# Performance work log

Measured on AMD Instinct MI355X. Metric: run time of the kernel, lower is better.

The kernel has to match this reference:

```python
import jax, jax.numpy as jnp
import numpy as np

EMBED = 1024
HEADS = 16
HEAD_DIM = EMBED // HEADS


def setup_inputs() -> dict:
    key = jax.random.key(0)
    ks = jax.random.split(key, 8)
    N, S = 4, 2048
    inp = {
        "values": jax.random.normal(ks[0], (N, S, EMBED), jnp.float32),
        "keys": jax.random.normal(ks[1], (N, S, EMBED), jnp.float32),
        "queries": jax.random.normal(ks[2], (N, S, EMBED), jnp.float32),
        "mask": jnp.ones((N, S), jnp.int32),  # unused by the original forward
        # learned params (torch Linear: y = x @ W.T + b)
        "Wv": jax.random.normal(ks[3], (HEAD_DIM, HEAD_DIM), jnp.float32) / np.sqrt(HEAD_DIM),
        "Wk": jax.random.normal(ks[4], (HEAD_DIM, HEAD_DIM), jnp.float32) / np.sqrt(HEAD_DIM),
        "Wq": jax.random.normal(ks[5], (HEAD_DIM, HEAD_DIM), jnp.float32) / np.sqrt(HEAD_DIM),
        "Wo": jax.random.normal(ks[6], (EMBED, EMBED), jnp.float32) / np.sqrt(EMBED),
        "bo": jax.random.normal(ks[7], (EMBED,), jnp.float32) * 0.01,
    }
    return inp


def reference(values, keys, queries, mask, Wv, Wk, Wq, Wo, bo):
    N, S, _ = queries.shape
    # reshape to (N, len, heads, head_dim)
    v = values.reshape(N, S, HEADS, HEAD_DIM)
    k = keys.reshape(N, S, HEADS, HEAD_DIM)
    q = queries.reshape(N, S, HEADS, HEAD_DIM)
    # per-head linear projections (weights shared across heads), y = x @ W.T
    v = jnp.einsum('nlhd,ed->nlhe', v, Wv)
    k = jnp.einsum('nlhd,ed->nlhe', k, Wk)
    q = jnp.einsum('nlhd,ed->nlhe', q, Wq)
    # attention scores scaled by sqrt(embed_size), faithful to original
    scores = jnp.einsum('nqhd,nkhd->nhqk', q, k) / jnp.sqrt(jnp.float32(EMBED))
    attn = jax.nn.softmax(scores, axis=3)
    out = jnp.einsum('nhql,nlhd->nqhd', attn, v).reshape(N, S, EMBED)
    return out @ Wo.T + bo
```

## Files before the change

kernel.cpp:

```cpp
#include <hip/hip_runtime.h>


using f32x4  = __attribute__((ext_vector_type(4))) float;
using f32x16 = __attribute__((ext_vector_type(16))) float;
using bf16x8 = __attribute__((ext_vector_type(8))) __bf16;
using u32x4  = __attribute__((ext_vector_type(4))) unsigned int;
using u16x8  = __attribute__((ext_vector_type(8))) unsigned short;
typedef unsigned short u16;
typedef unsigned int   u32;
typedef unsigned long long u64;

#define SEQ 2048
#define EMB 1024
#define NHEADS 16
#define HDIM 64
#define NBATCH 4
#define NH 64

__device__ __forceinline__ u16 f2bf(float f) {
  u32 u = __builtin_bit_cast(u32, f);
  return (u16)((u + 0x7fffu + ((u >> 16) & 1u)) >> 16);
}

__device__ __forceinline__ u32 cvtpk_bf16(float a, float b) {
  u32 d;
  asm("v_cvt_pk_bf16_f32 %0, %1, %2" : "=v"(d) : "v"(a), "v"(b));
  return d;
}

__device__ __forceinline__ f32x4 mfma16(bf16x8 a, bf16x8 b, f32x4 c) {
  return __builtin_amdgcn_mfma_f32_16x16x32_bf16(a, b, c, 0, 0, 0);
}

__device__ __forceinline__ f32x16 mfma32(bf16x8 a, bf16x8 b, f32x16 c) {
  return __builtin_amdgcn_mfma_f32_32x32x16_bf16(a, b, c, 0, 0, 0);
}

__device__ __forceinline__ bf16x8 cvt8(f32x4 a, f32x4 b) {
  u32x4 r;
  r[0] = cvtpk_bf16(a[0], a[1]);
  r[1] = cvtpk_bf16(a[2], a[3]);
  r[2] = cvtpk_bf16(b[0], b[1]);
  r[3] = cvtpk_bf16(b[2], b[3]);
  return __builtin_bit_cast(bf16x8, r);
}

__device__ __forceinline__ float fexp2(float x) {
#if __has_builtin(__builtin_amdgcn_exp2f)
  return __builtin_amdgcn_exp2f(x);
#else
  return __expf(x * 0.6931471805599453f);
#endif
}

__device__ __forceinline__ void swap_words(u32 a, u32 b, int hi, u32& wlo, u32& whi) {
#if __has_builtin(__builtin_amdgcn_permlane32_swap)
  (void)hi;
  auto rr = __builtin_amdgcn_permlane32_swap((int)a, (int)b, false, false);
  wlo = (u32)rr[0];
  whi = (u32)rr[1];
#else
  u32 pa = (u32)__shfl_xor((int)a, 32);
  u32 pb = (u32)__shfl_xor((int)b, 32);
  wlo = hi ? pb : a;
  whi = hi ? b : pa;
#endif
}

__global__ __launch_bounds__(256) void proj_kernel(
    const float* __restrict__ Xq, const float* __restrict__ Xk, const float* __restrict__ Xv,
    const float* __restrict__ Wq, const float* __restrict__ Wk, const float* __restrict__ Wv,
    u16* __restrict__ Qp, u16* __restrict__ Kp, u16* __restrict__ Vp)
{
  int which = blockIdx.y;
  const float* X = which == 0 ? Xq : (which == 1 ? Xk : Xv);
  const float* W = which == 0 ? Wq : (which == 1 ? Wk : Wv);
  u16* Out = which == 0 ? Qp : (which == 1 ? Kp : Vp);
  float wscale = which == 0 ? 0.045084220027780106f : 1.0f;

  __shared__ u16 Osm[64 * 72];

  int t = threadIdx.x;
  int w = t >> 6, l = t & 63, l15 = l & 15, grp = l >> 4;
  int g0 = blockIdx.x * 64;

  bf16x8 wf[4][2];
#pragma unroll
  for (int nt = 0; nt < 4; nt++) {
    int c = nt * 16 + l15;
#pragma unroll
    for (int dc = 0; dc < 2; dc++) {
      const float* p = W + c * 64 + dc * 32 + grp * 8;
      f32x4 a = *(const f32x4*)p;
      f32x4 b = *(const f32x4*)(p + 4);
      a *= wscale; b *= wscale;
      wf[nt][dc] = cvt8(a, b);
    }
  }
  int grow = g0 + w * 16 + l15;
  const float* xr = X + (long)grow * 64;
  bf16x8 af[2];
#pragma unroll
  for (int dc = 0; dc < 2; dc++) {
    f32x4 a = *(const f32x4*)(xr + dc * 32 + grp * 8);
    f32x4 b = *(const f32x4*)(xr + dc * 32 + grp * 8 + 4);
    af[dc] = cvt8(a, b);
  }
  f32x4 acc[4] = {};
#pragma unroll
  for (int dc = 0; dc < 2; dc++)
#pragma unroll
    for (int nt = 0; nt < 4; nt++)
      acc[nt] = mfma16(af[dc], wf[nt][dc], acc[nt]);

#pragma unroll
  for (int r = 0; r < 4; r++)
#pragma unroll
    for (int nt = 0; nt < 4; nt++)
      Osm[(w * 16 + grp * 4 + r) * 72 + nt * 16 + l15] = f2bf(acc[nt][r]);

  int rl = t >> 2, qtr = t & 3;
  const char* srcp = (const char*)Osm + rl * 144 + qtr * 32;
  u32x4 v0 = *(const u32x4*)srcp;
  u32x4 v1 = *(const u32x4*)(srcp + 16);
  int g = g0 + rl;
  int n = g >> 15, s = (g >> 4) & 2047, h = g & 15;
  char* dstp = (char*)(Out + (((long)(n * NHEADS + h) * SEQ + s) << 6)) + qtr * 32;
  *(u32x4*)dstp = v0;
  *(u32x4*)(dstp + 16) = v1;
}

__global__ __launch_bounds__(256) void transpose_v(
    const u16* __restrict__ Vp, u16* __restrict__ Vt)
{
  int st = blockIdx.x;
  int nh = blockIdx.y;
  __shared__ u16 Vs[64 * 65];
  int t = threadIdx.x;
  const u16* src = Vp + ((long)nh * SEQ + st * 64) * 64;
#pragma unroll
  for (int p = 0; p < 2; p++) {
    int row = p * 32 + (t >> 3);
    int c0 = (t & 7) * 8;
    u32x4 u = *(const u32x4*)(src + row * 64 + c0);
    u16x8 v = __builtin_bit_cast(u16x8, u);
#pragma unroll
    for (int j = 0; j < 8; j++) Vs[(c0 + j) * 65 + row] = v[j];
  }
  __syncthreads();
  int e = t >> 2, k0 = (t & 3) * 16;
  u16x8 lo, hi;
#pragma unroll
  for (int j = 0; j < 8; j++) { lo[j] = Vs[e * 65 + k0 + j]; hi[j] = Vs[e * 65 + k0 + 8 + j]; }
  u16* dst = Vt + ((long)nh * 64 + e) * SEQ + st * 64 + k0;
  *(u32x4*)dst = __builtin_bit_cast(u32x4, lo);
  *(u32x4*)(dst + 8) = __builtin_bit_cast(u32x4, hi);
}

__global__ __launch_bounds__(256) void conv_wo(
    const float* __restrict__ Wo, u16* __restrict__ Wob)
{
  int i = (blockIdx.x * 256 + threadIdx.x) * 4;
  f32x4 v = *(const f32x4*)(Wo + i);
  u32 w0 = cvtpk_bf16(v[0], v[1]);
  u32 w1 = cvtpk_bf16(v[2], v[3]);
  u64 pk = (u64)w0 | ((u64)w1 << 32);
  *(u64*)(Wob + i) = pk;
}


#define LDV(off) __builtin_bit_cast(bf16x8, *(const u32x4*)(smem + (off)))

#define ATTN_STEP(CUROFF, DOSTAGE, DOPREF) do {                            \
    f32x16 zz = {};                                                        \
    f32x16 s0, s1;                                                         \
    __builtin_amdgcn_s_setprio(1);                                         \
    {                                                                      \
      bf16x8 kf0 = LDV(koff[0] + (CUROFF));                                \
      bf16x8 kf1 = LDV(koff[1] + (CUROFF));                                \
      s0 = mfma32(kf0, qf[0], zz);                                         \
      s1 = mfma32(kf1, qf[0], zz);                                         \
    }                                                                      \
    _Pragma("unroll")                                                      \
    for (int dc = 1; dc < 4; dc++) {                                       \
      bf16x8 kf0 = LDV(koff[dc * 2 + 0] + (CUROFF));                       \
      bf16x8 kf1 = LDV(koff[dc * 2 + 1] + (CUROFF));                       \
      s0 = mfma32(kf0, qf[dc], s0);                                        \
      s1 = mfma32(kf1, qf[dc], s1);                                        \
    }                                                                      \
    __builtin_amdgcn_s_setprio(0);                                         \
    if (DOSTAGE) {                                                         \
      *(u32x4*)(smem + sphys0 + ((CUROFF) ^ 16384)) = kreg[0];             \
      *(u32x4*)(smem + sphys1 + ((CUROFF) ^ 16384)) = kreg[1];             \
      *(u32x4*)(smem + sphys0 + 8192 + ((CUROFF) ^ 16384)) = vreg[0];      \
      *(u32x4*)(smem + sphys1 + 8192 + ((CUROFF) ^ 16384)) = vreg[1];      \
      if (DOPREF) {                                                        \
        kreg[0] = *(const u32x4*)kp0; kp0 += 8192;                         \
        kreg[1] = *(const u32x4*)kp1; kp1 += 8192;                         \
        vreg[0] = *(const u32x4*)vp0; vp0 += 128;                          \
        vreg[1] = *(const u32x4*)vp1; vp1 += 128;                          \
      }                                                                    \
    }                                                                      \
                                    \
    _Pragma("unroll")                                                      \
    for (int r = 0; r < 16; r++) s0[r] = fexp2(s0[r]);                     \
    _Pragma("unroll")                                                      \
    for (int r = 0; r < 16; r++) s1[r] = fexp2(s1[r]);                     \
    { f32x16 ss = s0 + s1;                                                 \
      f32x4 q4 = { ss[0]+ss[4], ss[1]+ss[5], ss[2]+ss[6], ss[3]+ss[7] };   \
      f32x4 q5 = { ss[8]+ss[12], ss[9]+ss[13], ss[10]+ss[14], ss[11]+ss[15] }; \
      f32x4 q6 = q4 + q5;                                                  \
      lrun += (q6[0] + q6[1]) + (q6[2] + q6[3]); }                         \
              \
    bf16x8 pB[4];                                                          \
    { u32 xw[8], wq[16];                                                   \
      _Pragma("unroll")                                                    \
      for (int i = 0; i < 8; i++) xw[i] = cvtpk_bf16(s0[2*i], s0[2*i+1]);  \
      swap_words(xw[0], xw[2], hi, wq[0], wq[2]);                          \
      swap_words(xw[1], xw[3], hi, wq[1], wq[3]);                          \
      swap_words(xw[4], xw[6], hi, wq[4], wq[6]);                          \
      swap_words(xw[5], xw[7], hi, wq[5], wq[7]);                          \
      _Pragma("unroll")                                                    \
      for (int i = 0; i < 8; i++) xw[i] = cvtpk_bf16(s1[2*i], s1[2*i+1]);  \
      swap_words(xw[0], xw[2], hi, wq[8], wq[10]);                         \
      swap_words(xw[1], xw[3], hi, wq[9], wq[11]);                         \
      swap_words(xw[4], xw[6], hi, wq[12], wq[14]);                        \
      swap_words(xw[5], xw[7], hi, wq[13], wq[15]);                        \
      _Pragma("unroll")                                                    \
      for (int kb = 0; kb < 4; kb++) {                                     \
        u32x4 v4 = { wq[kb*4+0], wq[kb*4+1], wq[kb*4+2], wq[kb*4+3] };     \
        pB[kb] = __builtin_bit_cast(bf16x8, v4); } }                       \
                                                 \
    __builtin_amdgcn_s_setprio(1);                                         \
    _Pragma("unroll")                                                      \
    for (int kb = 0; kb < 4; kb++) {                                       \
      bf16x8 vf0 = LDV(koff[kb * 2 + 0] + 8192 + (CUROFF));                \
      bf16x8 vf1 = LDV(koff[kb * 2 + 1] + 8192 + (CUROFF));                \
      o0 = mfma32(vf0, pB[kb], o0);                                        \
      o1 = mfma32(vf1, pB[kb], o1);                                        \
    }                                                                      \
    __builtin_amdgcn_s_setprio(0);                                         \
    __syncthreads();                                                       \
  } while (0)

__global__ __launch_bounds__(256, 3) void attn_kernel(
    const u16* __restrict__ Qp, const u16* __restrict__ Kp, const u16* __restrict__ Vt,
    u16* __restrict__ AO)
{
  int nh = blockIdx.x;
  int qb = blockIdx.y;
  int n = nh >> 4, h = nh & 15;

  __shared__ __align__(16) char smem[32768];

  int t = threadIdx.x, w = t >> 6, l = t & 63;
  int l31 = l & 31, hi = l >> 5;

  long qrow = (long)nh * SEQ + qb * 128 + w * 32 + l31;
  const char* qbase = (const char*)Qp + qrow * 128;
  bf16x8 qf[4];
#pragma unroll
  for (int dc = 0; dc < 4; dc++)
    qf[dc] = __builtin_bit_cast(bf16x8, *(const u32x4*)(qbase + dc * 32 + hi * 16));

  f32x16 o0 = {}, o1 = {};
  float lrun = 0.f;

  int koff[8];
#pragma unroll
  for (int dc = 0; dc < 4; dc++)
#pragma unroll
    for (int half = 0; half < 2; half++) {
      int row = half * 32 + l31;
      int cc = dc * 2 + hi;
      koff[dc * 2 + half] = row * 128 + ((cc ^ (row & 7)) << 4);
    }

  int sr0 = t >> 3, sc = t & 7, sr1 = sr0 + 32;
  int sphys0 = sr0 * 128 + ((sc ^ (sr0 & 7)) << 4);
  int sphys1 = sr1 * 128 + ((sc ^ (sr1 & 7)) << 4);

  const char* Kg = (const char*)(Kp + (long)nh * SEQ * 64);
  const char* Vg = (const char*)(Vt + (long)nh * 64 * SEQ);
  const char* kp0 = Kg + sr0 * 128 + sc * 16;
  const char* kp1 = Kg + sr1 * 128 + sc * 16;
  const char* vp0 = Vg + (long)sr0 * 4096 + sc * 16;
  const char* vp1 = Vg + (long)sr1 * 4096 + sc * 16;

  u32x4 kreg[2], vreg[2];
  kreg[0] = *(const u32x4*)kp0;
  kreg[1] = *(const u32x4*)kp1;
  vreg[0] = *(const u32x4*)vp0;
  vreg[1] = *(const u32x4*)vp1;
  *(u32x4*)(smem + sphys0) = kreg[0];
  *(u32x4*)(smem + sphys1) = kreg[1];
  *(u32x4*)(smem + 8192 + sphys0) = vreg[0];
  *(u32x4*)(smem + 8192 + sphys1) = vreg[1];
  kreg[0] = *(const u32x4*)(kp0 + 8192); kp0 += 16384;
  kreg[1] = *(const u32x4*)(kp1 + 8192); kp1 += 16384;
  vreg[0] = *(const u32x4*)(vp0 + 128);  vp0 += 256;
  vreg[1] = *(const u32x4*)(vp1 + 128);  vp1 += 256;
  __syncthreads();

  for (int kt2 = 0; kt2 < 16; kt2++) {
    ATTN_STEP(0, true, (kt2 < 15));
    ATTN_STEP(16384, (kt2 < 15), (kt2 < 15));
  }

  lrun += __shfl_xor(lrun, 32);
  float inv = 1.0f / lrun;
  int qlocal = w * 32 + l31;
  char* OsmB = smem;
#pragma unroll
  for (int i = 0; i < 8; i++) {
    int e0 = ((2 * i) & 3) + 8 * ((2 * i) >> 2) + 4 * hi;
    *(u32*)(OsmB + qlocal * 144 + 2 * e0) = cvtpk_bf16(o0[2*i] * inv, o0[2*i+1] * inv);
    *(u32*)(OsmB + qlocal * 144 + 2 * (e0 + 32)) = cvtpk_bf16(o1[2*i] * inv, o1[2*i+1] * inv);
  }
  __syncthreads();
  int qr = t >> 1, half = t & 1;
  const char* src = OsmB + qr * 144 + half * 64;
  long qg = (long)qb * 128 + qr;
  char* dst = (char*)(AO + ((long)n * SEQ + qg) * EMB + h * 64 + half * 32);
#pragma unroll
  for (int j = 0; j < 4; j++)
    *(u32x4*)(dst + j * 16) = *(const u32x4*)(src + j * 16);
}

__global__ __launch_bounds__(256) void gemm_out(
    const u16* __restrict__ A, const u16* __restrict__ B,
    const float* __restrict__ bias, float* __restrict__ C)
{
  int bm0 = blockIdx.x;
  int bm = (bm0 & 7) * 8 + (bm0 >> 3);
  int bn = blockIdx.y;
  __shared__ __align__(16) char gsm[65536];
  int t = threadIdx.x, w = t >> 6, l = t & 63;
  int l31 = l & 31, hi = l >> 5;
  int wm = w >> 1, wn = w & 1;
  f32x16 acc[2][2] = {};
  const char* Ab = (const char*)(A + (long)bm * 128 * 1024);
  const char* Bb = (const char*)(B + (long)bn * 128 * 1024);

  int cphys[4];
  long cgoff[4];
#pragma unroll
  for (int p = 0; p < 4; p++) {
    int i = t + p * 256;
    int row = i >> 3, c = i & 7;
    cphys[p] = row * 128 + ((c ^ (row & 7)) << 4);
    cgoff[p] = (long)row * 2048 + c * 16;
  }

  int aoff[2][4], boff[2][4];
#pragma unroll
  for (int ti = 0; ti < 2; ti++)
#pragma unroll
    for (int kk = 0; kk < 4; kk++) {
      int rowa = wm * 64 + ti * 32 + l31;
      int rowb = wn * 64 + ti * 32 + l31;
      int c = kk * 2 + hi;
      aoff[ti][kk] = rowa * 128 + ((c ^ (rowa & 7)) << 4);
      boff[ti][kk] = 16384 + rowb * 128 + ((c ^ (rowb & 7)) << 4);
    }

  u32x4 areg[4], breg[4];
#pragma unroll
  for (int p = 0; p < 4; p++) {
    areg[p] = *(const u32x4*)(Ab + cgoff[p]);
    breg[p] = *(const u32x4*)(Bb + cgoff[p]);
  }
#pragma unroll
  for (int p = 0; p < 4; p++) {
    *(u32x4*)(gsm + cphys[p]) = areg[p];
    *(u32x4*)(gsm + 16384 + cphys[p]) = breg[p];
  }
#pragma unroll
  for (int p = 0; p < 4; p++) {
    areg[p] = *(const u32x4*)(Ab + cgoff[p] + 128);
    breg[p] = *(const u32x4*)(Bb + cgoff[p] + 128);
  }
  __syncthreads();

  for (int kt = 0; kt < 16; kt++) {
    const char* cur = gsm + ((kt & 1) << 15);
    char* nxt = gsm + (((kt + 1) & 1) << 15);

    if (kt + 1 < 16) {
#pragma unroll
      for (int p = 0; p < 4; p++) {
        *(u32x4*)(nxt + cphys[p]) = areg[p];
        *(u32x4*)(nxt + 16384 + cphys[p]) = breg[p];
      }
      if (kt + 2 < 16) {
#pragma unroll
        for (int p = 0; p < 4; p++) {
          areg[p] = *(const u32x4*)(Ab + cgoff[p] + (kt + 2) * 128);
          breg[p] = *(const u32x4*)(Bb + cgoff[p] + (kt + 2) * 128);
        }
      }
    }

    __builtin_amdgcn_s_setprio(1);
#pragma unroll
    for (int kk = 0; kk < 4; kk++) {
      bf16x8 af0 = __builtin_bit_cast(bf16x8, *(const u32x4*)(cur + aoff[0][kk]));
      bf16x8 af1 = __builtin_bit_cast(bf16x8, *(const u32x4*)(cur + aoff[1][kk]));
      bf16x8 bf0 = __builtin_bit_cast(bf16x8, *(const u32x4*)(cur + boff[0][kk]));
      bf16x8 bf1 = __builtin_bit_cast(bf16x8, *(const u32x4*)(cur + boff[1][kk]));
      acc[0][0] = mfma32(af0, bf0, acc[0][0]);
      acc[0][1] = mfma32(af0, bf1, acc[0][1]);
      acc[1][0] = mfma32(af1, bf0, acc[1][0]);
      acc[1][1] = mfma32(af1, bf1, acc[1][1]);
    }
    __builtin_amdgcn_s_setprio(0);

    __syncthreads();
  }

  float bv[2];
#pragma unroll
  for (int tj = 0; tj < 2; tj++) bv[tj] = bias[bn * 128 + wn * 64 + tj * 32 + l31];
#pragma unroll
  for (int ti = 0; ti < 2; ti++)
#pragma unroll
    for (int tj = 0; tj < 2; tj++) {
#pragma unroll
      for (int r = 0; r < 16; r++) {
        long row = (long)bm * 128 + wm * 64 + ti * 32 + ((r & 3) + 8 * (r >> 2) + 4 * hi);
        C[row * 1024 + bn * 128 + wn * 64 + tj * 32 + l31] = acc[ti][tj][r] + bv[tj];
      }
    }
}

extern "C" void kernel_launch(void* const* d_in, const int* in_sizes, int n_in,
                              void* d_out, int out_size, void* d_ws, size_t ws_size,
                              hipStream_t stream)
{
  const float* Vx = (const float*)d_in[0];
  const float* Kx = (const float*)d_in[1];
  const float* Qx = (const float*)d_in[2];
  const float* Wv = (const float*)d_in[4];
  const float* Wk = (const float*)d_in[5];
  const float* Wq = (const float*)d_in[6];
  const float* Wo = (const float*)d_in[7];
  const float* bo = (const float*)d_in[8];
  float* out = (float*)d_out;
  char* ws = (char*)d_ws;

  u16* Qp  = (u16*)(ws);
  u16* Kp  = (u16*)(ws + (1L << 24));
  u16* Vt  = (u16*)(ws + (2L << 24));
  u16* Vp  = (u16*)(ws + (3L << 24));
  u16* AO  = Vp;
  u16* Wob = (u16*)(ws + (4L << 24));

  proj_kernel<<<dim3(2048, 3), 256, 0, stream>>>(Qx, Kx, Vx, Wq, Wk, Wv, Qp, Kp, Vp);
  transpose_v<<<dim3(32, 64), 256, 0, stream>>>(Vp, Vt);
  conv_wo<<<1024, 256, 0, stream>>>(Wo, Wob);
  attn_kernel<<<dim3(64, 16), 256, 0, stream>>>(Qp, Kp, Vt, AO);
  gemm_out<<<dim3(64, 8), 256, 0, stream>>>(AO, Wob, bo, out);
}
```

Baseline: 174.6 us.

## Double attention query tile to 256 rows with 512-thread blocks

Each attention block now handles 256 query rows with 8 waves instead of 128 rows with 4 waves. Every thread stages one K/V chunk per tile instead of two, so each K/V tile loaded into LDS serves twice as many queries and global K/V traffic drops. The exp2 is also replaced with inline v_exp_f32 assembly. In exchange, launch bounds of (512,4) force a tight register budget that may cause spills, and the grid shrinks to 512 blocks.

New measurement: 197.4 us. 1.13x slower.

```diff
diff --git a/kernel.cpp b/kernel.cpp
--- a/kernel.cpp
+++ b/kernel.cpp
@@ -46,11 +46,9 @@
 }
 
 __device__ __forceinline__ float fexp2(float x) {
-#if __has_builtin(__builtin_amdgcn_exp2f)
-  return __builtin_amdgcn_exp2f(x);
-#else
-  return __expf(x * 0.6931471805599453f);
-#endif
+  float r;
+  asm("v_exp_f32 %0, %1" : "=v"(r) : "v"(x));
+  return r;
 }
 
 __device__ __forceinline__ void swap_words(u32 a, u32 b, int hi, u32& wlo, u32& whi) {
@@ -190,15 +188,11 @@
     }                                                                      \
     __builtin_amdgcn_s_setprio(0);                                         \
     if (DOSTAGE) {                                                         \
-      *(u32x4*)(smem + sphys0 + ((CUROFF) ^ 16384)) = kreg[0];             \
-      *(u32x4*)(smem + sphys1 + ((CUROFF) ^ 16384)) = kreg[1];             \
-      *(u32x4*)(smem + sphys0 + 8192 + ((CUROFF) ^ 16384)) = vreg[0];      \
-      *(u32x4*)(smem + sphys1 + 8192 + ((CUROFF) ^ 16384)) = vreg[1];      \
+      *(u32x4*)(smem + sphys + ((CUROFF) ^ 16384)) = kreg;                 \
+      *(u32x4*)(smem + sphys + 8192 + ((CUROFF) ^ 16384)) = vreg;          \
       if (DOPREF) {                                                        \
-        kreg[0] = *(const u32x4*)kp0; kp0 += 8192;                         \
-        kreg[1] = *(const u32x4*)kp1; kp1 += 8192;                         \
-        vreg[0] = *(const u32x4*)vp0; vp0 += 128;                          \
-        vreg[1] = *(const u32x4*)vp1; vp1 += 128;                          \
+        kreg = *(const u32x4*)kp; kp += 8192;                              \
+        vreg = *(const u32x4*)vp; vp += 128;                               \
       }                                                                    \
     }                                                                      \
                                     \
@@ -243,7 +237,7 @@
     __syncthreads();                                                       \
   } while (0)
 
-__global__ __launch_bounds__(256, 3) void attn_kernel(
+__global__ __launch_bounds__(512, 4) void attn_kernel(
     const u16* __restrict__ Qp, const u16* __restrict__ Kp, const u16* __restrict__ Vt,
     u16* __restrict__ AO)
 {
@@ -251,12 +245,12 @@
   int qb = blockIdx.y;
   int n = nh >> 4, h = nh & 15;
 
-  __shared__ __align__(16) char smem[32768];
+  __shared__ __align__(16) char smem[36864];
 
   int t = threadIdx.x, w = t >> 6, l = t & 63;
   int l31 = l & 31, hi = l >> 5;
 
-  long qrow = (long)nh * SEQ + qb * 128 + w * 32 + l31;
+  long qrow = (long)nh * SEQ + qb * 256 + w * 32 + l31;
   const char* qbase = (const char*)Qp + qrow * 128;
   bf16x8 qf[4];
 #pragma unroll
@@ -276,30 +270,21 @@
       koff[dc * 2 + half] = row * 128 + ((cc ^ (row & 7)) << 4);
     }
 
-  int sr0 = t >> 3, sc = t & 7, sr1 = sr0 + 32;
-  int sphys0 = sr0 * 128 + ((sc ^ (sr0 & 7)) << 4);
-  int sphys1 = sr1 * 128 + ((sc ^ (sr1 & 7)) << 4);
+  int sr = t >> 3, sc = t & 7;
+  int sphys = sr * 128 + ((sc ^ (sr & 7)) << 4);
 
   const char* Kg = (const char*)(Kp + (long)nh * SEQ * 64);
   const char* Vg = (const char*)(Vt + (long)nh * 64 * SEQ);
-  const char* kp0 = Kg + sr0 * 128 + sc * 16;
-  const char* kp1 = Kg + sr1 * 128 + sc * 16;
-  const char* vp0 = Vg + (long)sr0 * 4096 + sc * 16;
-  const char* vp1 = Vg + (long)sr1 * 4096 + sc * 16;
-
-  u32x4 kreg[2], vreg[2];
-  kreg[0] = *(const u32x4*)kp0;
-  kreg[1] = *(const u32x4*)kp1;
-  vreg[0] = *(const u32x4*)vp0;
-  vreg[1] = *(const u32x4*)vp1;
-  *(u32x4*)(smem + sphys0) = kreg[0];
-  *(u32x4*)(smem + sphys1) = kreg[1];
-  *(u32x4*)(smem + 8192 + sphys0) = vreg[0];
-  *(u32x4*)(smem + 8192 + sphys1) = vreg[1];
-  kreg[0] = *(const u32x4*)(kp0 + 8192); kp0 += 16384;
-  kreg[1] = *(const u32x4*)(kp1 + 8192); kp1 += 16384;
-  vreg[0] = *(const u32x4*)(vp0 + 128);  vp0 += 256;
-  vreg[1] = *(const u32x4*)(vp1 + 128);  vp1 += 256;
+  const char* kp = Kg + sr * 128 + sc * 16;
+  const char* vp = Vg + (long)sr * 4096 + sc * 16;
+
+  u32x4 kreg, vreg;
+  kreg = *(const u32x4*)kp;
+  vreg = *(const u32x4*)vp;
+  *(u32x4*)(smem + sphys) = kreg;
+  *(u32x4*)(smem + 8192 + sphys) = vreg;
+  kreg = *(const u32x4*)(kp + 8192); kp += 16384;
+  vreg = *(const u32x4*)(vp + 128);  vp += 256;
   __syncthreads();
 
   for (int kt2 = 0; kt2 < 16; kt2++) {
@@ -320,7 +305,7 @@
   __syncthreads();
   int qr = t >> 1, half = t & 1;
   const char* src = OsmB + qr * 144 + half * 64;
-  long qg = (long)qb * 128 + qr;
+  long qg = (long)qb * 256 + qr;
   char* dst = (char*)(AO + ((long)n * SEQ + qg) * EMB + h * 64 + half * 32);
 #pragma unroll
   for (int j = 0; j < 4; j++)
@@ -458,6 +443,6 @@
   proj_kernel<<<dim3(2048, 3), 256, 0, stream>>>(Qx, Kx, Vx, Wq, Wk, Wv, Qp, Kp, Vp);
   transpose_v<<<dim3(32, 64), 256, 0, stream>>>(Vp, Vt);
   conv_wo<<<1024, 256, 0, stream>>>(Wo, Wob);
-  attn_kernel<<<dim3(64, 16), 256, 0, stream>>>(Qp, Kp, Vt, AO);
+  attn_kernel<<<dim3(64, 8), 512, 0, stream>>>(Qp, Kp, Vt, AO);
   gemm_out<<<dim3(64, 8), 256, 0, stream>>>(AO, Wob, bo, out);
 }
```
